# Optimization experiments

Hardware: AMD Instinct MI355X
Metric: run time of the kernel (lower is better)

Reference implementation:

```python
import jax, jax.numpy as jnp
import numpy as np

NUM_NODES = 2
ALPHA = 1.0
BETA = 5.0
KL_BETA = 1.0
LOG_2PI = float(np.log(2.0 * np.pi))

K_COMP = 8192   # number of KDE components / empirical samples
N_SAMP = 8192   # n_samples drawn from the KDE
B_X = 2048      # x_data batch
D_W = NUM_NODES * NUM_NODES + 4 * NUM_NODES + 1  # 13 weights per sample


def setup_inputs() -> dict:
    key = jax.random.key(0)
    k1, k2, k3, k4, k5 = jax.random.split(key, 5)
    return {
        "emp_samples": jax.random.normal(k1, (K_COMP, D_W), dtype=jnp.float32),
        "log_kde_rhos": jnp.zeros((K_COMP,), dtype=jnp.float32),
        "x": jax.random.normal(k2, (B_X, 1), dtype=jnp.float32),
        "y": jax.random.normal(k3, (B_X,), dtype=jnp.float32),
        "eps": jax.random.normal(k4, (N_SAMP, D_W), dtype=jnp.float32),
        "rand_idxs": jax.random.randint(k5, (N_SAMP,), 0, K_COMP, dtype=jnp.int64 if jax.config.jax_enable_x64 else jnp.int32),
    }


def _batch_regression(w, x):
    # w: [N, 13], x: [B, 1] -> y_preds [N, B]
    n = NUM_NODES
    i = 0
    w1 = w[:, i:i + n]; i += n                                   # [N, n]
    b1 = w[:, i:i + n]; i += n                                   # [N, n]
    w2 = w[:, i:i + n * n].reshape(-1, n, n); i += n * n         # [N, n, n]
    b2 = w[:, i:i + n]; i += n                                   # [N, n]
    w3 = w[:, i:i + n]; i += n                                   # [N, n]
    b3 = w[:, i]                                                 # [N]
    h = jnp.einsum('bi,kj->bki', w1, x) + b1[:, None, :]         # [N, B, n]
    h = jnp.tanh(h)
    h = jnp.einsum('bij,bkj->bki', w2, h) + b2[:, None, :]
    h = jnp.tanh(h)
    return jnp.einsum('bi,bki->bk', w3, h) + b3[:, None]         # [N, B]


def reference(emp_samples, log_kde_rhos, x, y, eps, rand_idxs):
    kde_std = jax.nn.softplus(log_kde_rhos)                      # [K]
    kde_var = kde_std * kde_std                                  # [K]
    # sample_from_kde (noise externalized)
    w = emp_samples[rand_idxs] + eps * kde_std[rand_idxs][:, None]  # [N, D]
    # data likelihood: Normal(y_pred, 1/sqrt(beta))
    y_preds = _batch_regression(w, x)                            # [N, B]
    ll = -0.5 * BETA * (y_preds - y[None, :]) ** 2 + 0.5 * (jnp.log(BETA) - LOG_2PI)
    data_lp = ll.sum(-1).mean()
    # weight prior: Normal(0, 1/sqrt(alpha)), sum over weight dim
    prior_lp = (-0.5 * ALPHA * w * w + 0.5 * (jnp.log(ALPHA) - LOG_2PI)).sum(1)  # [N]
    # KDE mixture log-prob: isotropic Gaussian components, uniform weights
    d = w.shape[1]
    sq = (jnp.sum(w * w, axis=1)[:, None]
          - 2.0 * (w @ emp_samples.T)
          + jnp.sum(emp_samples * emp_samples, axis=1)[None, :])  # [N, K]
    comp_lp = -0.5 * (d * LOG_2PI + d * jnp.log(kde_var)[None, :] + sq / kde_var[None, :])
    q_lp = jax.scipy.special.logsumexp(comp_lp, axis=1) - jnp.log(jnp.float32(emp_samples.shape[0]))  # [N]
    kl_term = (q_lp - prior_lp).mean()
    return data_lp - KL_BETA * kl_term
```

## Files before the change

### kernel.cpp

```cpp
#include <hip/hip_runtime.h>
#include <math.h>

#define KCOMP 8192
#define NSAMP 8192
#define BX 2048
#define DW 13

#define LOG2PI  1.8378770664093453f
#define LOGBETA 1.6094379124341003f
#define LOGK    9.0109131020929380f
#define LOG2E   1.4426950408889634f
#define LN2     0.6931471805599453f
#define C2E     2.8853900817779268f

#define NBLK_KL   1024
#define NBLK_DATA 512
#define NBLK_MONO (NBLK_KL + NBLK_DATA)

#define NK     512
#define XLO    (-4.75f)
#define DXK    (9.5f / (float)NK)
#define USCALE ((float)NK / 9.5f)

typedef __attribute__((ext_vector_type(8))) short bf16x8_t;
typedef __attribute__((ext_vector_type(4))) float f32x4_t;

__device__ __forceinline__ float fast_log(float x) {
    return __builtin_amdgcn_logf(x) * LN2;
}
__device__ __forceinline__ float softplus_stable(float x) {
    return fmaxf(x, 0.0f) + log1pf(expf(-fabsf(x)));
}
__device__ __forceinline__ unsigned short to_bf16(float f) {
    unsigned int u = __builtin_bit_cast(unsigned int, f);
    u += 0x7FFFu + ((u >> 16) & 1u);
    return (unsigned short)(u >> 16);
}
__device__ __forceinline__ float from_bf16(unsigned short h) {
    unsigned int u = ((unsigned int)h) << 16;
    return __builtin_bit_cast(float, u);
}
__device__ __forceinline__ void tanh_pair(float a0, float a1, float& t0, float& t1) {
    float e0 = __builtin_amdgcn_exp2f(a0);
    float e1 = __builtin_amdgcn_exp2f(a1);
    float d0 = e0 + 1.0f, d1 = e1 + 1.0f;
    float inv = __builtin_amdgcn_rcpf(d0 * d1);
    t0 = fmaf(-2.0f, d1 * inv, 1.0f);
    t1 = fmaf(-2.0f, d0 * inv, 1.0f);
}

#define OFF_PART  0
#define OFF_RSUM  2048
#define OFF_G2    10240
#define OFF_A2    18432
#define OFF_HQ    26624
#define OFF_PL    34816
#define OFF_WF    43008
#define OFF_WB    174080
#define OFF_EMPB  305152
#define OFF_STATP 436224
#define OFF_STATL 436800
#define OFF_STATC 437376
#define OFF_SYY   437952

__global__ __launch_bounds__(256) void prep_kernel(
        const float* __restrict__ emp, const float* __restrict__ rhos,
        const float* __restrict__ eps, const int* __restrict__ idxs,
        const float* __restrict__ x, const float* __restrict__ y,
        float* __restrict__ ws) {
    __shared__ float sb[5 * NK];
    __shared__ float sred[4];
    int tid = threadIdx.x;

    if (blockIdx.x < 64) {
        int g = blockIdx.x * 256 + tid;
        if (g < KCOMP) {
            int j = g;
            ws[OFF_RSUM + j] = 0.0f;
            unsigned short* empB = (unsigned short*)(ws + OFF_EMPB);
            float sp  = softplus_stable(rhos[j]);
            float var = sp * sp;
            float inv = 1.0f / var;
            float esq = 0.0f;
            #pragma unroll
            for (int c = 0; c < DW; ++c) {
                float e = emp[j * DW + c];
                esq = fmaf(e, e, esq);
                unsigned short eb = to_bf16(e);
                empB[j * 32 + c]      = eb;
                empB[j * 32 + 16 + c] = eb;
            }
            #pragma unroll
            for (int c = DW; c < 16; ++c) { empB[j*32+c] = 0; empB[j*32+16+c] = 0; }
            float f1v = -6.5f * (LOG2PI + logf(var)) - 0.5f * esq * inv;
            ws[OFF_G2 + j] = inv * LOG2E;
            ws[OFF_A2 + j] = f1v * LOG2E;
        } else {
            int b  = g - KCOMP;
            int i0 = idxs[b];
            unsigned short* wB = (unsigned short*)(ws + OFF_WB);
            float* wF = ws + OFF_WF;
            float sp  = softplus_stable(rhos[i0]);
            float var = sp * sp;
            float inv = 1.0f / var;
            float esq = 0.0f, wsq = 0.0f, dot = 0.0f;
            #pragma unroll
            for (int c = 0; c < DW; ++c) {
                float e  = emp[i0 * DW + c];
                float wc = fmaf(eps[b * DW + c], sp, e);
                esq = fmaf(e, e, esq);
                wsq = fmaf(wc, wc, wsq);
                dot = fmaf(wc, e, dot);
                wF[b * 16 + c] = wc;
                unsigned short hi = to_bf16(wc);
                wB[b * 32 + c]      = hi;
                wB[b * 32 + 16 + c] = to_bf16(wc - from_bf16(hi));
            }
            #pragma unroll
            for (int c = DW; c < 16; ++c) { wF[b*16+c] = 0.0f; wB[b*32+c] = 0; wB[b*32+16+c] = 0; }
            float f1v = -6.5f * (LOG2PI + logf(var)) - 0.5f * esq * inv;
            float h   = 0.5f * wsq;
            ws[OFF_HQ + b] = h;
            ws[OFF_PL + b] = fmaf(inv, dot - h, f1v) * LOG2E;
        }
        return;
    }

    float* sS11 = sb;
    float* sSff = sb + NK;
    float* sS1f = sb + 2 * NK;
    float* sS1y = sb + 3 * NK;
    float* sSfy = sb + 4 * NK;
    for (int i = tid; i < 5 * NK; i += 256) sb[i] = 0.0f;
    __syncthreads();

    float syy = 0.0f;
    for (int p = tid; p < BX; p += 256) {
        float xv = x[p], yv = y[p];
        float u = fmaf(xv, USCALE, (float)(NK / 2));
        u = fminf(fmaxf(u, 0.0f), (float)NK - 0.001f);
        int   i = (int)u;
        float f = u - (float)i;
        float g1 = 1.0f - f;
        atomicAdd(&sS11[i], g1 * g1);
        atomicAdd(&sSff[i], f * f);
        atomicAdd(&sS1f[i], g1 * f);
        atomicAdd(&sS1y[i], g1 * yv);
        atomicAdd(&sSfy[i], f * yv);
        syy = fmaf(yv, yv, syy);
    }
    __syncthreads();

    for (int j = tid; j < 576; j += 256) {
        float pj = 0.0f, lj = 0.0f, cj = 0.0f;
        if (j < NK)            { pj  = sS11[j];     lj  = sS1y[j];     cj = 2.0f * sS1f[j]; }
        if (j >= 1 && j <= NK) { pj += sSff[j - 1]; lj += sSfy[j - 1]; }
        ws[OFF_STATP + j] = pj;
        ws[OFF_STATL + j] = -2.0f * lj;
        ws[OFF_STATC + j] = cj;
    }

    int wv = tid >> 6, ln = tid & 63;
    #pragma unroll
    for (int o = 32; o; o >>= 1) syy += __shfl_down(syy, o);
    if (ln == 0) sred[wv] = syy;
    __syncthreads();
    if (tid == 0) ws[OFF_SYY] = sred[0] + sred[1] + sred[2] + sred[3];
}

__global__ __launch_bounds__(256) void main_kernel(float* __restrict__ ws) {
    __shared__ float red[4];
    int tid = threadIdx.x, wave = tid >> 6, lane = tid & 63;

    float* part = ws + OFF_PART;
    float* rsum = ws + OFF_RSUM;
    const float* G2  = ws + OFF_G2;
    const float* A2  = ws + OFF_A2;
    const float* hqA = ws + OFF_HQ;
    const float* plA = ws + OFF_PL;
    const float* wF  = ws + OFF_WF;
    const unsigned short* wB   = (const unsigned short*)(ws + OFF_WB);
    const unsigned short* empB = (const unsigned short*)(ws + OFF_EMPB);

    if (blockIdx.x >= NBLK_KL) {
        int d = blockIdx.x - NBLK_KL;
        const float* statP = ws + OFF_STATP;
        const float* statL = ws + OFF_STATL;
        const float* statC = ws + OFF_STATC;

        float P[9], L[9], C[9];
        #pragma unroll
        for (int t = 0; t < 9; ++t) {
            int j = t * 64 + lane;
            P[t] = statP[j];
            L[t] = statL[j];
            C[t] = statC[j];
        }

        float q = 0.0f;
        int row0 = (d * 4 + wave) * 4;
        #pragma unroll 1
        for (int rr = 0; rr < 4; ++rr) {
            int row = row0 + rr;
            const float4* wr = (const float4*)(wF + row * 16);
            float4 wa = wr[0], wbv = wr[1], wcv = wr[2], wdv = wr[3];
            float s0 = wa.x * C2E, s1 = wa.y * C2E, s2 = wa.z * C2E, s3 = wa.w * C2E;
            float s4 = wbv.x * C2E, s5 = wbv.y * C2E, s6 = wbv.z * C2E, s7 = wbv.w * C2E;
            float s8 = wcv.x * C2E, s9 = wcv.y * C2E;
            float w10 = wcv.z, w11 = wcv.w, w12 = wdv.x;

            float k[10];
            #pragma unroll
            for (int t = 0; t < 9; ++t) {
                float xk = fmaf((float)(t * 64 + lane), DXK, XLO);
                float h10, h11, h20, h21;
                tanh_pair(fmaf(s0, xk, s2), fmaf(s1, xk, s3), h10, h11);
                tanh_pair(fmaf(s4, h10, fmaf(s5, h11, s8)),
                          fmaf(s6, h10, fmaf(s7, h11, s9)), h20, h21);
                k[t] = fmaf(w10, h20, fmaf(w11, h21, w12));
            }
            k[9] = k[0];

            #pragma unroll
            for (int t = 0; t < 9; ++t) {
                float a   = k[t];
                float an  = __shfl(k[t], (lane + 1) & 63);
                float an0 = __shfl(k[t + 1], 0);
                an = (lane == 63) ? an0 : an;
                float tq = fmaf(a, P[t], L[t]);
                tq = fmaf(an, C[t], tq);
                q = fmaf(a, tq, q);
            }
        }
        #pragma unroll
        for (int o = 32; o; o >>= 1) q += __shfl_down(q, o);
        if (lane == 0) red[wave] = q;
        __syncthreads();
        if (tid == 0) part[d] = red[0] + red[1] + red[2] + red[3];
    } else {
        int bid     = blockIdx.x;
        int rowtile = bid & 127;
        int chunk   = bid >> 7;
        int rowbase = rowtile * 64 + wave * 16;
        int half = lane >> 4;
        int m16  = lane & 15;

        const bf16x8_t afrag = *(const bf16x8_t*)(wB + (rowbase + m16) * 32 + half * 8);
        float h[4], p[4];
        #pragma unroll
        for (int r = 0; r < 4; ++r) {
            h[r] = hqA[rowbase + half * 4 + r];
            p[r] = plA[rowbase + half * 4 + r];
        }
        float s[4] = {0.f, 0.f, 0.f, 0.f};

        int j0 = chunk * (KCOMP / 8);
        #pragma unroll 2
        for (int jt = 0; jt < (KCOMP / 8) / 16; ++jt) {
            int j = j0 + jt * 16 + m16;
            bf16x8_t bfrag = *(const bf16x8_t*)(empB + j * 32 + half * 8);
            f32x4_t c = {0.f, 0.f, 0.f, 0.f};
            c = __builtin_amdgcn_mfma_f32_16x16x32_bf16(afrag, bfrag, c, 0, 0, 0);
            float g2 = G2[j], a2 = A2[j];
            #pragma unroll
            for (int r = 0; r < 4; ++r) {
                float t = fmaf(-g2, h[r], a2 - p[r]);
                s[r] += __builtin_amdgcn_exp2f(fmaf(g2, c[r], t));
            }
        }
        #pragma unroll
        for (int r = 0; r < 4; ++r) {
            float S = s[r];
            S += __shfl_xor(S, 1); S += __shfl_xor(S, 2);
            S += __shfl_xor(S, 4); S += __shfl_xor(S, 8);
            if (m16 == 0) atomicAdd(&rsum[rowbase + half * 4 + r], S);
        }
    }
}

__global__ __launch_bounds__(1024) void fin_kernel(
        const float* __restrict__ ws, float* __restrict__ out) {
    __shared__ float red1[16], red2[16];
    int tid = threadIdx.x, wave = tid >> 6, lane = tid & 63;

    const float* part = ws + OFF_PART;
    const float* rsum = ws + OFF_RSUM;
    const float* hqA  = ws + OFF_HQ;
    const float* plA  = ws + OFF_PL;

    float s1 = 0.0f;
    for (int i = tid; i < NBLK_DATA; i += 1024) s1 += part[i];
    float s2 = 0.0f;
    for (int b = tid; b < NSAMP; b += 1024) {
        float q     = plA[b] * LN2 + fast_log(rsum[b]) - LOGK;
        float prior = -hqA[b] - 6.5f * LOG2PI;
        s2 += q - prior;
    }
    #pragma unroll
    for (int o = 32; o; o >>= 1) { s1 += __shfl_down(s1, o); s2 += __shfl_down(s2, o); }
    if (lane == 0) { red1[wave] = s1; red2[wave] = s2; }
    __syncthreads();
    if (tid < 16) {
        s1 = red1[tid]; s2 = red2[tid];
        #pragma unroll
        for (int o = 8; o; o >>= 1) { s1 += __shfl_down(s1, o); s2 += __shfl_down(s2, o); }
        if (tid == 0) {
            float syy = ws[OFF_SYY];
            float data_lp = -2.5f * (s1 / (float)NSAMP + syy)
                            + (float)BX * 0.5f * (LOGBETA - LOG2PI);
            out[0] = data_lp - s2 / (float)NSAMP;
        }
    }
}

extern "C" void kernel_launch(void* const* d_in, const int* in_sizes, int n_in,
                              void* d_out, int out_size, void* d_ws, size_t ws_size,
                              hipStream_t stream) {
    const float* emp  = (const float*)d_in[0];
    const float* rhos = (const float*)d_in[1];
    const float* x    = (const float*)d_in[2];
    const float* y    = (const float*)d_in[3];
    const float* eps  = (const float*)d_in[4];
    const int*   idxs = (const int*)d_in[5];
    float* out = (float*)d_out;
    float* ws  = (float*)d_ws;

    prep_kernel<<<65, 256, 0, stream>>>(emp, rhos, eps, idxs, x, y, ws);
    main_kernel<<<NBLK_MONO, 256, 0, stream>>>(ws);
    fin_kernel<<<1, 1024, 0, stream>>>(ws, out);
}
```

Measured before the change: 107.2 us.

## Give each data-term wave one row with contiguous knots; widen prep grid

The data-likelihood blocks now handle one sample row per wave instead of four. Each lane owns eight consecutive spline knots, so the neighbour-knot coupling needs no cross-lane shuffles, and the stats tables are loaded with float4 reads. The data-term block count goes up fourfold to spread the work across more CUs. The prep kernel moves to 64-thread blocks with more blocks, which removes the shared-memory reduction for syy. The trade is more blocks with more launch and reduction overhead, and the partial-sum buffer must hold 2048 entries.

```diff
diff --git a/kernel.cpp b/kernel.cpp
--- a/kernel.cpp
+++ b/kernel.cpp
@@ -14,7 +14,7 @@
 #define C2E     2.8853900817779268f
 
 #define NBLK_KL   1024
-#define NBLK_DATA 512
+#define NBLK_DATA 2048
 #define NBLK_MONO (NBLK_KL + NBLK_DATA)
 
 #define NK     512
@@ -63,17 +63,16 @@
 #define OFF_STATC 437376
 #define OFF_SYY   437952
 
-__global__ __launch_bounds__(256) void prep_kernel(
+__global__ __launch_bounds__(64) void prep_kernel(
         const float* __restrict__ emp, const float* __restrict__ rhos,
         const float* __restrict__ eps, const int* __restrict__ idxs,
         const float* __restrict__ x, const float* __restrict__ y,
         float* __restrict__ ws) {
     __shared__ float sb[5 * NK];
-    __shared__ float sred[4];
     int tid = threadIdx.x;
 
-    if (blockIdx.x < 64) {
-        int g = blockIdx.x * 256 + tid;
+    if (blockIdx.x < 256) {
+        int g = blockIdx.x * 64 + tid;
         if (g < KCOMP) {
             int j = g;
             ws[OFF_RSUM + j] = 0.0f;
@@ -131,11 +130,11 @@
     float* sS1f = sb + 2 * NK;
     float* sS1y = sb + 3 * NK;
     float* sSfy = sb + 4 * NK;
-    for (int i = tid; i < 5 * NK; i += 256) sb[i] = 0.0f;
+    for (int i = tid; i < 5 * NK; i += 64) sb[i] = 0.0f;
     __syncthreads();
 
     float syy = 0.0f;
-    for (int p = tid; p < BX; p += 256) {
+    for (int p = tid; p < BX; p += 64) {
         float xv = x[p], yv = y[p];
         float u = fmaf(xv, USCALE, (float)(NK / 2));
         u = fminf(fmaxf(u, 0.0f), (float)NK - 0.001f);
@@ -151,7 +150,7 @@
     }
     __syncthreads();
 
-    for (int j = tid; j < 576; j += 256) {
+    for (int j = tid; j < 576; j += 64) {
         float pj = 0.0f, lj = 0.0f, cj = 0.0f;
         if (j < NK)            { pj  = sS11[j];     lj  = sS1y[j];     cj = 2.0f * sS1f[j]; }
         if (j >= 1 && j <= NK) { pj += sSff[j - 1]; lj += sSfy[j - 1]; }
@@ -160,12 +159,9 @@
         ws[OFF_STATC + j] = cj;
     }
 
-    int wv = tid >> 6, ln = tid & 63;
     #pragma unroll
     for (int o = 32; o; o >>= 1) syy += __shfl_down(syy, o);
-    if (ln == 0) sred[wv] = syy;
-    __syncthreads();
-    if (tid == 0) ws[OFF_SYY] = sred[0] + sred[1] + sred[2] + sred[3];
+    if (tid == 0) ws[OFF_SYY] = syy;
 }
 
 __global__ __launch_bounds__(256) void main_kernel(float* __restrict__ ws) {
@@ -188,50 +184,48 @@
         const float* statL = ws + OFF_STATL;
         const float* statC = ws + OFF_STATC;
 
-        float P[9], L[9], C[9];
-        #pragma unroll
-        for (int t = 0; t < 9; ++t) {
-            int j = t * 64 + lane;
-            P[t] = statP[j];
-            L[t] = statL[j];
-            C[t] = statC[j];
-        }
-
+        int j0 = lane * 8;
+        float4 Pa = *(const float4*)(statP + j0);
+        float4 Pb = *(const float4*)(statP + j0 + 4);
+        float  P8 = statP[j0 + 8];
+        float4 La = *(const float4*)(statL + j0);
+        float4 Lb = *(const float4*)(statL + j0 + 4);
+        float  L8 = statL[j0 + 8];
+        float4 Ca = *(const float4*)(statC + j0);
+        float4 Cb = *(const float4*)(statC + j0 + 4);
+
+        int row = d * 4 + wave;
+        const float4* wr = (const float4*)(wF + row * 16);
+        float4 wa = wr[0], wbv = wr[1], wcv = wr[2], wdv = wr[3];
+        float s0 = wa.x * C2E, s1 = wa.y * C2E, s2 = wa.z * C2E, s3 = wa.w * C2E;
+        float s4 = wbv.x * C2E, s5 = wbv.y * C2E, s6 = wbv.z * C2E, s7 = wbv.w * C2E;
+        float s8 = wcv.x * C2E, s9 = wcv.y * C2E;
+        float w10 = wcv.z, w11 = wcv.w, w12 = wdv.x;
+
+        float k[9];
+        #pragma unroll
+        for (int i = 0; i < 9; ++i) {
+            float xk = fmaf((float)(j0 + i), DXK, XLO);
+            float h10, h11, h20, h21;
+            tanh_pair(fmaf(s0, xk, s2), fmaf(s1, xk, s3), h10, h11);
+            tanh_pair(fmaf(s4, h10, fmaf(s5, h11, s8)),
+                      fmaf(s6, h10, fmaf(s7, h11, s9)), h20, h21);
+            k[i] = fmaf(w10, h20, fmaf(w11, h21, w12));
+        }
+
+        float Pv[8] = {Pa.x, Pa.y, Pa.z, Pa.w, Pb.x, Pb.y, Pb.z, Pb.w};
+        float Lv[8] = {La.x, La.y, La.z, La.w, Lb.x, Lb.y, Lb.z, Lb.w};
+        float Cv[8] = {Ca.x, Ca.y, Ca.z, Ca.w, Cb.x, Cb.y, Cb.z, Cb.w};
         float q = 0.0f;
-        int row0 = (d * 4 + wave) * 4;
-        #pragma unroll 1
-        for (int rr = 0; rr < 4; ++rr) {
-            int row = row0 + rr;
-            const float4* wr = (const float4*)(wF + row * 16);
-            float4 wa = wr[0], wbv = wr[1], wcv = wr[2], wdv = wr[3];
-            float s0 = wa.x * C2E, s1 = wa.y * C2E, s2 = wa.z * C2E, s3 = wa.w * C2E;
-            float s4 = wbv.x * C2E, s5 = wbv.y * C2E, s6 = wbv.z * C2E, s7 = wbv.w * C2E;
-            float s8 = wcv.x * C2E, s9 = wcv.y * C2E;
-            float w10 = wcv.z, w11 = wcv.w, w12 = wdv.x;
-
-            float k[10];
-            #pragma unroll
-            for (int t = 0; t < 9; ++t) {
-                float xk = fmaf((float)(t * 64 + lane), DXK, XLO);
-                float h10, h11, h20, h21;
-                tanh_pair(fmaf(s0, xk, s2), fmaf(s1, xk, s3), h10, h11);
-                tanh_pair(fmaf(s4, h10, fmaf(s5, h11, s8)),
-                          fmaf(s6, h10, fmaf(s7, h11, s9)), h20, h21);
-                k[t] = fmaf(w10, h20, fmaf(w11, h21, w12));
-            }
-            k[9] = k[0];
-
-            #pragma unroll
-            for (int t = 0; t < 9; ++t) {
-                float a   = k[t];
-                float an  = __shfl(k[t], (lane + 1) & 63);
-                float an0 = __shfl(k[t + 1], 0);
-                an = (lane == 63) ? an0 : an;
-                float tq = fmaf(a, P[t], L[t]);
-                tq = fmaf(an, C[t], tq);
-                q = fmaf(a, tq, q);
-            }
-        }
+        #pragma unroll
+        for (int i = 0; i < 8; ++i) {
+            float t = fmaf(k[i], Pv[i], Lv[i]);
+            t = fmaf(k[i + 1], Cv[i], t);
+            q = fmaf(k[i], t, q);
+        }
+        float lm = (lane == 63) ? k[8] : 0.0f;
+        q = fmaf(lm, fmaf(k[8], P8, L8), q);
+
         #pragma unroll
         for (int o = 32; o; o >>= 1) q += __shfl_down(q, o);
         if (lane == 0) red[wave] = q;
@@ -325,7 +319,7 @@
     float* out = (float*)d_out;
     float* ws  = (float*)d_ws;
 
-    prep_kernel<<<65, 256, 0, stream>>>(emp, rhos, eps, idxs, x, y, ws);
+    prep_kernel<<<257, 64, 0, stream>>>(emp, rhos, eps, idxs, x, y, ws);
     main_kernel<<<NBLK_MONO, 256, 0, stream>>>(ws);
     fin_kernel<<<1, 1024, 0, stream>>>(ws, out);
 }
```

New measurement: 112.6 us. 1.05x slower.
